# Optimization experiments

Measured on AMD Instinct MI355X. Metric: run time of the kernel, lower is better.

Reference implementation:

```python
import jax, jax.numpy as jnp
import numpy as np

VOCAB = 77
BLANK = VOCAB          # blank_index=-1 in tf.nn.ctc_greedy_decoder -> last class (77)
PRED_LEN = 30          # ctc_prediction_len


def _greedy_decode_row(best):
    """CTC greedy decode of one row. best: [T] int32 argmax path.
    Collapse consecutive repeats, drop blanks, pad to PRED_LEN with -1
    (matches tf.nn.ctc_greedy_decoder + sparse_to_dense(default=-1))."""
    prev = jnp.concatenate([jnp.full((1,), -1, best.dtype), best[:-1]])
    keep = (best != BLANK) & (best != prev)
    pos = jnp.cumsum(keep.astype(jnp.int32)) - 1
    # route dropped / overflow tokens to a scratch slot PRED_LEN
    pos = jnp.where(keep, jnp.minimum(pos, PRED_LEN), PRED_LEN)
    out = jnp.full((PRED_LEN + 1,), -1, jnp.int32).at[pos].set(best)
    return out[:PRED_LEN]


def setup_inputs() -> dict:
    key = jax.random.key(0)
    k1, k2, k3 = jax.random.split(key, 3)
    B, T, D = 1024, 80, 512
    feat_vec = jax.random.normal(k1, (B, T, D), jnp.float32)
    W = jax.random.normal(k2, (D, VOCAB + 1), jnp.float32) * (1.0 / np.sqrt(D))
    b = jnp.zeros((VOCAB + 1,), jnp.float32)
    y = jax.random.randint(k3, (B, PRED_LEN), 0, VOCAB)
    times = T
    return {"feat_vec": feat_vec, "W": W, "b": b, "y": y, "times": times}


def reference(feat_vec, W, b, y, times):
    # Dense classifier with softmax: [B, T, VOCAB+1]
    logits = jax.nn.softmax(jnp.einsum("btd,dc->btc", feat_vec, W) + b, axis=-1)
    # CTC greedy decode (merge_repeated=True), full sequence length = times = T
    best = jnp.argmax(logits, axis=-1).astype(jnp.int32)  # [B, T]
    res_lab = jax.vmap(_greedy_decode_row)(best)          # [B, PRED_LEN]
    return logits, res_lab
```

## Files before the change

### kernel.cpp

```cpp
#include <hip/hip_runtime.h>
#include <math.h>

#define B_     1024
#define T_     80
#define D_     512
#define C_     78
#define PRED_  30
#define BLANK_ 77
#define NKK    16
#define FRAG   512
#define PLANE_STRIDE (5 * NKK * FRAG)
#define ROWS_PB 160

typedef __attribute__((ext_vector_type(8))) _Float16 f16x8;
typedef __attribute__((ext_vector_type(4))) float    f32x4;

__device__ __forceinline__ void load_lds16(const void* g, void* l) {
    __builtin_amdgcn_global_load_lds(
        (const __attribute__((address_space(1))) unsigned int*)g,
        (__attribute__((address_space(3))) unsigned int*)l, 16, 0, 0);
}

__global__ __launch_bounds__(256) void prep_w(const float* __restrict__ W,
                                              ushort* __restrict__ Wf) {
    int i = blockIdx.x * 256 + threadIdx.x;
    if (i >= 2 * PLANE_STRIDE) return;
    int j    = i & 7;
    int lane = (i >> 3) & 63;
    int kk   = (i >> 9) & 15;
    int rest = i >> 13;
    int ct   = rest % 5;
    int plane = rest / 5;
    int q = lane >> 4, n = lane & 15;
    int k = kk * 32 + q * 8 + j;
    int c = ct * 16 + n;
    float v = (c < C_) ? W[k * C_ + c] : 0.f;
    _Float16 h1 = (_Float16)v;
    union { _Float16 h; ushort u; } cv;
    cv.h = (plane == 0) ? h1 : (_Float16)(v - (float)h1);
    Wf[i] = cv.u;
}

__global__ __launch_bounds__(320, 3) void gemm_ctc(
    const float* __restrict__ feat,
    const ushort* __restrict__ Wf,
    const float* __restrict__ bias,
    float* __restrict__ probs,
    float* __restrict__ lab)
{
    __shared__ __align__(16) float Abuf[2][ROWS_PB * 32];
    __shared__ int best_s[2][T_];

    const int tid  = threadIdx.x;
    const int w    = tid >> 6;
    const int lane = tid & 63;
    const int q    = lane >> 4;
    const int n    = lane & 15;

    f32x4 acc[2][5];
    #pragma unroll
    for (int t = 0; t < 2; ++t)
        #pragma unroll
        for (int ct = 0; ct < 5; ++ct)
            acc[t][ct] = (f32x4){0.f, 0.f, 0.f, 0.f};

    const float*  Abase = feat + (size_t)blockIdx.x * ROWS_PB * D_;
    const ushort* bp0   = Wf + lane * 8;

    auto stage = [&](int buf, int kk) {
        #pragma unroll
        for (int r = 0; r < 4; ++r) {
            int p   = r * 320 + w * 64 + lane;
            int row = p >> 3;
            int pc  = p & 7;
            int src = pc ^ (row & 7);
            const float* g = Abase + (size_t)row * D_ + kk * 32 + src * 4;
            float* l = &Abuf[buf][(size_t)(r * 320 + w * 64) * 4];
            load_lds16(g, l);
        }
    };

    stage(0, 0);
    int cur = 0;
    for (int kk = 0; kk < NKK; ++kk) {
        __syncthreads();
        if (kk < NKK - 1) stage(cur ^ 1, kk + 1);

        const float* Ab = &Abuf[cur][0];
        f16x8 a1f[2], a2f[2];
        #pragma unroll
        for (int t = 0; t < 2; ++t) {
            int rowl = w * 32 + t * 16 + n;
            int sw   = n & 7;
            float4 f0 = *(const float4*)(Ab + rowl * 32 + (((2 * q)     ^ sw) * 4));
            float4 f1 = *(const float4*)(Ab + rowl * 32 + (((2 * q + 1) ^ sw) * 4));
            float v[8] = {f0.x, f0.y, f0.z, f0.w, f1.x, f1.y, f1.z, f1.w};
            #pragma unroll
            for (int j = 0; j < 8; ++j) {
                _Float16 h = (_Float16)v[j];
                a1f[t][j] = h;
                a2f[t][j] = (_Float16)(v[j] - (float)h);
            }
        }
        #pragma unroll
        for (int ct = 0; ct < 5; ++ct) {
            const ushort* bp = bp0 + (ct * NKK + kk) * FRAG;
            f16x8 b1 = *(const f16x8*)bp;
            f16x8 b2 = *(const f16x8*)(bp + PLANE_STRIDE);
            acc[0][ct] = __builtin_amdgcn_mfma_f32_16x16x32_f16(a1f[0], b1, acc[0][ct], 0, 0, 0);
            acc[0][ct] = __builtin_amdgcn_mfma_f32_16x16x32_f16(a2f[0], b1, acc[0][ct], 0, 0, 0);
            acc[0][ct] = __builtin_amdgcn_mfma_f32_16x16x32_f16(a1f[0], b2, acc[0][ct], 0, 0, 0);
            acc[0][ct] = __builtin_amdgcn_mfma_f32_16x16x32_f16(a2f[0], b2, acc[0][ct], 0, 0, 0);
            acc[1][ct] = __builtin_amdgcn_mfma_f32_16x16x32_f16(a1f[1], b1, acc[1][ct], 0, 0, 0);
            acc[1][ct] = __builtin_amdgcn_mfma_f32_16x16x32_f16(a2f[1], b1, acc[1][ct], 0, 0, 0);
            acc[1][ct] = __builtin_amdgcn_mfma_f32_16x16x32_f16(a1f[1], b2, acc[1][ct], 0, 0, 0);
            acc[1][ct] = __builtin_amdgcn_mfma_f32_16x16x32_f16(a2f[1], b2, acc[1][ct], 0, 0, 0);
        }
        cur ^= 1;
    }

    #pragma unroll
    for (int t = 0; t < 2; ++t) {
        float x[5][4];
        #pragma unroll
        for (int ct = 0; ct < 5; ++ct) {
            int c = ct * 16 + n;
            bool valid = (c < C_);
            float bv = valid ? bias[c] : 0.f;
            #pragma unroll
            for (int r = 0; r < 4; ++r)
                x[ct][r] = valid ? (acc[t][ct][r] + bv) : -INFINITY;
        }
        float av[4]; int ai[4];
        #pragma unroll
        for (int r = 0; r < 4; ++r) {
            av[r] = x[0][r]; ai[r] = n;
            #pragma unroll
            for (int ct = 1; ct < 5; ++ct) {
                int c = ct * 16 + n;
                if (x[ct][r] > av[r]) { av[r] = x[ct][r]; ai[r] = c; }
            }
        }
        #pragma unroll
        for (int off = 8; off >= 1; off >>= 1) {
            #pragma unroll
            for (int r = 0; r < 4; ++r) {
                float ov = __shfl_xor(av[r], off, 16);
                int   oi = __shfl_xor(ai[r], off, 16);
                if (ov > av[r] || (ov == av[r] && oi < ai[r])) { av[r] = ov; ai[r] = oi; }
            }
        }
        float s[4] = {0.f, 0.f, 0.f, 0.f};
        #pragma unroll
        for (int ct = 0; ct < 5; ++ct)
            #pragma unroll
            for (int r = 0; r < 4; ++r) {
                x[ct][r] = __expf(x[ct][r] - av[r]);
                s[r] += x[ct][r];
            }
        #pragma unroll
        for (int off = 8; off >= 1; off >>= 1)
            #pragma unroll
            for (int r = 0; r < 4; ++r) s[r] += __shfl_xor(s[r], off, 16);

        const size_t growb = (size_t)blockIdx.x * ROWS_PB + w * 32 + t * 16 + q * 4;
        #pragma unroll
        for (int r = 0; r < 4; ++r) {
            float inv = 1.f / s[r];
            float* op = probs + (growb + r) * C_;
            #pragma unroll
            for (int ct = 0; ct < 5; ++ct) {
                int c = ct * 16 + n;
                if (c < C_) __builtin_nontemporal_store(x[ct][r] * inv, op + c);
            }
        }
        if (n == 0) {
            int rl = w * 32 + t * 16 + q * 4;
            #pragma unroll
            for (int r = 0; r < 4; ++r) {
                int rr = rl + r;
                best_s[rr / T_][rr % T_] = ai[r];
            }
        }
    }
    __syncthreads();

    if (tid < 2) {
        const int* bs = best_s[tid];
        float* op = lab + ((size_t)blockIdx.x * 2 + tid) * PRED_;
        int prev = -1, pos = 0;
        for (int t2 = 0; t2 < T_; ++t2) {
            int v = bs[t2];
            if (v != BLANK_ && v != prev) {
                if (pos < PRED_) op[pos] = (float)v;
                ++pos;
            }
            prev = v;
        }
        for (int i2 = (pos < PRED_ ? pos : PRED_); i2 < PRED_; ++i2) op[i2] = -1.f;
    }
}

extern "C" void kernel_launch(void* const* d_in, const int* in_sizes, int n_in,
                              void* d_out, int out_size, void* d_ws, size_t ws_size,
                              hipStream_t stream) {
    const float* feat = (const float*)d_in[0];
    const float* W    = (const float*)d_in[1];
    const float* bias = (const float*)d_in[2];
    float*  probs = (float*)d_out;
    float*  lab   = probs + (size_t)B_ * T_ * C_;
    ushort* Wf    = (ushort*)d_ws;

    hipLaunchKernelGGL(prep_w, dim3(320), dim3(256), 0, stream, W, Wf);
    hipLaunchKernelGGL(gemm_ctc, dim3(B_ / 2), dim3(320), 0, stream,
                       feat, Wf, bias, probs, lab);
}
```

Baseline: 263.2 us.

## Load A directly into registers, one sequence per block, drop lo*lo MFMA

Removes the LDS double-buffered staging of feature rows and instead has each lane load its A fragment straight from global memory with a one-step register prefetch. Each block now handles one sequence (80 rows, 16 per wave) instead of two, which doubles the grid and raises the occupancy hint. It also drops the low-times-low split-precision MFMA term, cutting matrix work by a quarter at a small accuracy cost. Without LDS staging, global loads are less coalesced (each lane reads 32 bytes across strided rows), and B fragments are reloaded per 16 rows instead of per 32.

```diff
diff --git a/kernel.cpp b/kernel.cpp
--- a/kernel.cpp
+++ b/kernel.cpp
@@ -10,16 +10,9 @@
 #define NKK    16
 #define FRAG   512
 #define PLANE_STRIDE (5 * NKK * FRAG)
-#define ROWS_PB 160
 
 typedef __attribute__((ext_vector_type(8))) _Float16 f16x8;
 typedef __attribute__((ext_vector_type(4))) float    f32x4;
-
-__device__ __forceinline__ void load_lds16(const void* g, void* l) {
-    __builtin_amdgcn_global_load_lds(
-        (const __attribute__((address_space(1))) unsigned int*)g,
-        (__attribute__((address_space(3))) unsigned int*)l, 16, 0, 0);
-}
 
 __global__ __launch_bounds__(256) void prep_w(const float* __restrict__ W,
                                               ushort* __restrict__ Wf) {
@@ -41,15 +34,14 @@
     Wf[i] = cv.u;
 }
 
-__global__ __launch_bounds__(320, 3) void gemm_ctc(
+__global__ __launch_bounds__(320, 4) void gemm_ctc(
     const float* __restrict__ feat,
     const ushort* __restrict__ Wf,
     const float* __restrict__ bias,
     float* __restrict__ probs,
     float* __restrict__ lab)
 {
-    __shared__ __align__(16) float Abuf[2][ROWS_PB * 32];
-    __shared__ int best_s[2][T_];
+    __shared__ int best_s[T_];
 
     const int tid  = threadIdx.x;
     const int w    = tid >> 6;
@@ -57,140 +49,111 @@
     const int q    = lane >> 4;
     const int n    = lane & 15;
 
-    f32x4 acc[2][5];
+    f32x4 acc[5];
     #pragma unroll
-    for (int t = 0; t < 2; ++t)
+    for (int ct = 0; ct < 5; ++ct)
+        acc[ct] = (f32x4){0.f, 0.f, 0.f, 0.f};
+
+    const float*  Ap  = feat + ((size_t)blockIdx.x * T_ + w * 16 + n) * D_ + q * 8;
+    const ushort* bp0 = Wf + lane * 8;
+
+    float4 c0 = *(const float4*)(Ap);
+    float4 c1 = *(const float4*)(Ap + 4);
+
+    #pragma unroll 2
+    for (int kk = 0; kk < NKK; ++kk) {
+        const int nk = (kk < NKK - 1) ? kk + 1 : NKK - 1;
+        float4 n0 = *(const float4*)(Ap + nk * 32);
+        float4 n1 = *(const float4*)(Ap + nk * 32 + 4);
+
+        float v[8] = {c0.x, c0.y, c0.z, c0.w, c1.x, c1.y, c1.z, c1.w};
+        f16x8 a1f, a2f;
         #pragma unroll
-        for (int ct = 0; ct < 5; ++ct)
-            acc[t][ct] = (f32x4){0.f, 0.f, 0.f, 0.f};
+        for (int j = 0; j < 8; ++j) {
+            _Float16 h = (_Float16)v[j];
+            a1f[j] = h;
+            a2f[j] = (_Float16)(v[j] - (float)h);
+        }
 
-    const float*  Abase = feat + (size_t)blockIdx.x * ROWS_PB * D_;
-    const ushort* bp0   = Wf + lane * 8;
+        const ushort* bpk = bp0 + kk * FRAG;
+        #pragma unroll
+        for (int ct = 0; ct < 5; ++ct) {
+            const ushort* bp = bpk + ct * (NKK * FRAG);
+            f16x8 b1 = *(const f16x8*)bp;
+            f16x8 b2 = *(const f16x8*)(bp + PLANE_STRIDE);
+            acc[ct] = __builtin_amdgcn_mfma_f32_16x16x32_f16(a1f, b1, acc[ct], 0, 0, 0);
+            acc[ct] = __builtin_amdgcn_mfma_f32_16x16x32_f16(a2f, b1, acc[ct], 0, 0, 0);
+            acc[ct] = __builtin_amdgcn_mfma_f32_16x16x32_f16(a1f, b2, acc[ct], 0, 0, 0);
+        }
+        c0 = n0; c1 = n1;
+    }
 
-    auto stage = [&](int buf, int kk) {
+    float x[5][4];
+    #pragma unroll
+    for (int ct = 0; ct < 5; ++ct) {
+        int c = ct * 16 + n;
+        bool valid = (c < C_);
+        float bv = valid ? bias[c] : 0.f;
+        #pragma unroll
+        for (int r = 0; r < 4; ++r)
+            x[ct][r] = valid ? (acc[ct][r] + bv) : -INFINITY;
+    }
+    float av[4]; int ai[4];
+    #pragma unroll
+    for (int r = 0; r < 4; ++r) {
+        av[r] = x[0][r]; ai[r] = n;
+        #pragma unroll
+        for (int ct = 1; ct < 5; ++ct) {
+            int c = ct * 16 + n;
+            if (x[ct][r] > av[r]) { av[r] = x[ct][r]; ai[r] = c; }
+        }
+    }
+    #pragma unroll
+    for (int off = 8; off >= 1; off >>= 1) {
         #pragma unroll
         for (int r = 0; r < 4; ++r) {
-            int p   = r * 320 + w * 64 + lane;
-            int row = p >> 3;
-            int pc  = p & 7;
-            int src = pc ^ (row & 7);
-            const float* g = Abase + (size_t)row * D_ + kk * 32 + src * 4;
-            float* l = &Abuf[buf][(size_t)(r * 320 + w * 64) * 4];
-            load_lds16(g, l);
+            float ov = __shfl_xor(av[r], off, 16);
+            int   oi = __shfl_xor(ai[r], off, 16);
+            if (ov > av[r] || (ov == av[r] && oi < ai[r])) { av[r] = ov; ai[r] = oi; }
         }
-    };
+    }
+    float s[4] = {0.f, 0.f, 0.f, 0.f};
+    #pragma unroll
+    for (int ct = 0; ct < 5; ++ct)
+        #pragma unroll
+        for (int r = 0; r < 4; ++r) {
+            x[ct][r] = __expf(x[ct][r] - av[r]);
+            s[r] += x[ct][r];
+        }
+    #pragma unroll
+    for (int off = 8; off >= 1; off >>= 1)
+        #pragma unroll
+        for (int r = 0; r < 4; ++r) s[r] += __shfl_xor(s[r], off, 16);
 
-    stage(0, 0);
-    int cur = 0;
-    for (int kk = 0; kk < NKK; ++kk) {
-        __syncthreads();
-        if (kk < NKK - 1) stage(cur ^ 1, kk + 1);
-
-        const float* Ab = &Abuf[cur][0];
-        f16x8 a1f[2], a2f[2];
-        #pragma unroll
-        for (int t = 0; t < 2; ++t) {
-            int rowl = w * 32 + t * 16 + n;
-            int sw   = n & 7;
-            float4 f0 = *(const float4*)(Ab + rowl * 32 + (((2 * q)     ^ sw) * 4));
-            float4 f1 = *(const float4*)(Ab + rowl * 32 + (((2 * q + 1) ^ sw) * 4));
-            float v[8] = {f0.x, f0.y, f0.z, f0.w, f1.x, f1.y, f1.z, f1.w};
-            #pragma unroll
-            for (int j = 0; j < 8; ++j) {
-                _Float16 h = (_Float16)v[j];
-                a1f[t][j] = h;
-                a2f[t][j] = (_Float16)(v[j] - (float)h);
-            }
-        }
-        #pragma unroll
-        for (int ct = 0; ct < 5; ++ct) {
-            const ushort* bp = bp0 + (ct * NKK + kk) * FRAG;
-            f16x8 b1 = *(const f16x8*)bp;
-            f16x8 b2 = *(const f16x8*)(bp + PLANE_STRIDE);
-            acc[0][ct] = __builtin_amdgcn_mfma_f32_16x16x32_f16(a1f[0], b1, acc[0][ct], 0, 0, 0);
-            acc[0][ct] = __builtin_amdgcn_mfma_f32_16x16x32_f16(a2f[0], b1, acc[0][ct], 0, 0, 0);
-            acc[0][ct] = __builtin_amdgcn_mfma_f32_16x16x32_f16(a1f[0], b2, acc[0][ct], 0, 0, 0);
-            acc[0][ct] = __builtin_amdgcn_mfma_f32_16x16x32_f16(a2f[0], b2, acc[0][ct], 0, 0, 0);
-            acc[1][ct] = __builtin_amdgcn_mfma_f32_16x16x32_f16(a1f[1], b1, acc[1][ct], 0, 0, 0);
-            acc[1][ct] = __builtin_amdgcn_mfma_f32_16x16x32_f16(a2f[1], b1, acc[1][ct], 0, 0, 0);
-            acc[1][ct] = __builtin_amdgcn_mfma_f32_16x16x32_f16(a1f[1], b2, acc[1][ct], 0, 0, 0);
-            acc[1][ct] = __builtin_amdgcn_mfma_f32_16x16x32_f16(a2f[1], b2, acc[1][ct], 0, 0, 0);
-        }
-        cur ^= 1;
-    }
-
+    const size_t growb = (size_t)blockIdx.x * T_ + w * 16 + q * 4;
     #pragma unroll
-    for (int t = 0; t < 2; ++t) {
-        float x[5][4];
+    for (int r = 0; r < 4; ++r) {
+        float inv = 1.f / s[r];
+        float* op = probs + (growb + r) * C_;
         #pragma unroll
         for (int ct = 0; ct < 5; ++ct) {
             int c = ct * 16 + n;
-            bool valid = (c < C_);
-            float bv = valid ? bias[c] : 0.f;
-            #pragma unroll
-            for (int r = 0; r < 4; ++r)
-                x[ct][r] = valid ? (acc[t][ct][r] + bv) : -INFINITY;
+            if (c < C_) __builtin_nontemporal_store(x[ct][r] * inv, op + c);
         }
-        float av[4]; int ai[4];
+    }
+    if (n == 0) {
+        int rl = w * 16 + q * 4;
         #pragma unroll
-        for (int r = 0; r < 4; ++r) {
-            av[r] = x[0][r]; ai[r] = n;
-            #pragma unroll
-            for (int ct = 1; ct < 5; ++ct) {
-                int c = ct * 16 + n;
-                if (x[ct][r] > av[r]) { av[r] = x[ct][r]; ai[r] = c; }
-            }
-        }
-        #pragma unroll
-        for (int off = 8; off >= 1; off >>= 1) {
-            #pragma unroll
-            for (int r = 0; r < 4; ++r) {
-                float ov = __shfl_xor(av[r], off, 16);
-                int   oi = __shfl_xor(ai[r], off, 16);
-                if (ov > av[r] || (ov == av[r] && oi < ai[r])) { av[r] = ov; ai[r] = oi; }
-            }
-        }
-        float s[4] = {0.f, 0.f, 0.f, 0.f};
-        #pragma unroll
-        for (int ct = 0; ct < 5; ++ct)
-            #pragma unroll
-            for (int r = 0; r < 4; ++r) {
-                x[ct][r] = __expf(x[ct][r] - av[r]);
-                s[r] += x[ct][r];
-            }
-        #pragma unroll
-        for (int off = 8; off >= 1; off >>= 1)
-            #pragma unroll
-            for (int r = 0; r < 4; ++r) s[r] += __shfl_xor(s[r], off, 16);
-
-        const size_t growb = (size_t)blockIdx.x * ROWS_PB + w * 32 + t * 16 + q * 4;
-        #pragma unroll
-        for (int r = 0; r < 4; ++r) {
-            float inv = 1.f / s[r];
-            float* op = probs + (growb + r) * C_;
-            #pragma unroll
-            for (int ct = 0; ct < 5; ++ct) {
-                int c = ct * 16 + n;
-                if (c < C_) __builtin_nontemporal_store(x[ct][r] * inv, op + c);
-            }
-        }
-        if (n == 0) {
-            int rl = w * 32 + t * 16 + q * 4;
-            #pragma unroll
-            for (int r = 0; r < 4; ++r) {
-                int rr = rl + r;
-                best_s[rr / T_][rr % T_] = ai[r];
-            }
-        }
+        for (int r = 0; r < 4; ++r)
+            best_s[rl + r] = ai[r];
     }
     __syncthreads();
 
-    if (tid < 2) {
-        const int* bs = best_s[tid];
-        float* op = lab + ((size_t)blockIdx.x * 2 + tid) * PRED_;
+    if (tid == 0) {
+        float* op = lab + (size_t)blockIdx.x * PRED_;
         int prev = -1, pos = 0;
         for (int t2 = 0; t2 < T_; ++t2) {
-            int v = bs[t2];
+            int v = best_s[t2];
             if (v != BLANK_ && v != prev) {
                 if (pos < PRED_) op[pos] = (float)v;
                 ++pos;
@@ -212,6 +175,6 @@
     ushort* Wf    = (ushort*)d_ws;
 
     hipLaunchKernelGGL(prep_w, dim3(320), dim3(256), 0, stream, W, Wf);
-    hipLaunchKernelGGL(gemm_ctc, dim3(B_ / 2), dim3(320), 0, stream,
+    hipLaunchKernelGGL(gemm_ctc, dim3(B_), dim3(320), 0, stream,
                        feat, Wf, bias, probs, lab);
 }
```

Result: slower. 284.5 us (+8.1%).

## Triple-buffer A and W fragments in LDS and drop lo*lo MFMA term

Applied to the files above, without the earlier changes.

W fragments are now staged into LDS alongside the feature tile through direct global-to-LDS loads, replacing per-wave global loads inside the K loop. The pipeline becomes triple-buffered, with explicit vmcnt waits and raw s_barrier instead of __syncthreads. The smallest split-fp16 correction product (a_lo*b_lo) is removed, cutting MFMAs by a quarter at a tiny accuracy cost. LDS use grows to about 92KB per block and the occupancy hint is removed, so far fewer blocks fit per CU, which may hurt latency hiding.

```diff
diff --git a/kernel.cpp b/kernel.cpp
--- a/kernel.cpp
+++ b/kernel.cpp
@@ -11,9 +11,13 @@
 #define FRAG   512
 #define PLANE_STRIDE (5 * NKK * FRAG)
 #define ROWS_PB 160
+#define A_BYTES (ROWS_PB * 128)
+#define SLICE_BYTES (A_BYTES + 10 * 1024)
 
 typedef __attribute__((ext_vector_type(8))) _Float16 f16x8;
 typedef __attribute__((ext_vector_type(4))) float    f32x4;
+
+#define WAITVM(N) asm volatile("s_waitcnt vmcnt(" #N ")" ::: "memory")
 
 __device__ __forceinline__ void load_lds16(const void* g, void* l) {
     __builtin_amdgcn_global_load_lds(
@@ -41,14 +45,14 @@
     Wf[i] = cv.u;
 }
 
-__global__ __launch_bounds__(320, 3) void gemm_ctc(
+__global__ __launch_bounds__(320) void gemm_ctc(
     const float* __restrict__ feat,
     const ushort* __restrict__ Wf,
     const float* __restrict__ bias,
     float* __restrict__ probs,
     float* __restrict__ lab)
 {
-    __shared__ __align__(16) float Abuf[2][ROWS_PB * 32];
+    __shared__ __align__(16) unsigned char Sbuf[3][SLICE_BYTES];
     __shared__ int best_s[2][T_];
 
     const int tid  = threadIdx.x;
@@ -57,6 +61,28 @@
     const int q    = lane >> 4;
     const int n    = lane & 15;
 
+    const float* Abase = feat + (size_t)blockIdx.x * ROWS_PB * D_;
+
+    auto stage = [&](int buf, int kk) {
+        #pragma unroll
+        for (int l = 0; l < 4; ++l) {
+            int rb  = w * 4 + l;
+            int row = rb * 8 + (lane >> 3);
+            int pc  = lane & 7;
+            int sc  = pc ^ (row & 7);
+            const float* g = Abase + (size_t)row * D_ + kk * 32 + sc * 4;
+            load_lds16(g, Sbuf[buf] + rb * 1024);
+        }
+        #pragma unroll
+        for (int f2 = 0; f2 < 2; ++f2) {
+            int f     = w * 2 + f2;
+            int plane = f / 5, ct = f % 5;
+            const ushort* g = Wf + (size_t)plane * PLANE_STRIDE
+                                 + (ct * NKK + kk) * FRAG + lane * 8;
+            load_lds16(g, Sbuf[buf] + A_BYTES + f * 1024);
+        }
+    };
+
     f32x4 acc[2][5];
     #pragma unroll
     for (int t = 0; t < 2; ++t)
@@ -64,29 +90,9 @@
         for (int ct = 0; ct < 5; ++ct)
             acc[t][ct] = (f32x4){0.f, 0.f, 0.f, 0.f};
 
-    const float*  Abase = feat + (size_t)blockIdx.x * ROWS_PB * D_;
-    const ushort* bp0   = Wf + lane * 8;
-
-    auto stage = [&](int buf, int kk) {
-        #pragma unroll
-        for (int r = 0; r < 4; ++r) {
-            int p   = r * 320 + w * 64 + lane;
-            int row = p >> 3;
-            int pc  = p & 7;
-            int src = pc ^ (row & 7);
-            const float* g = Abase + (size_t)row * D_ + kk * 32 + src * 4;
-            float* l = &Abuf[buf][(size_t)(r * 320 + w * 64) * 4];
-            load_lds16(g, l);
-        }
-    };
-
-    stage(0, 0);
-    int cur = 0;
-    for (int kk = 0; kk < NKK; ++kk) {
-        __syncthreads();
-        if (kk < NKK - 1) stage(cur ^ 1, kk + 1);
-
-        const float* Ab = &Abuf[cur][0];
+    auto body = [&](int buf) {
+        const float*  Ab = (const float*)(Sbuf[buf]);
+        const ushort* Bb = (const ushort*)(Sbuf[buf] + A_BYTES);
         f16x8 a1f[2], a2f[2];
         #pragma unroll
         for (int t = 0; t < 2; ++t) {
@@ -104,20 +110,29 @@
         }
         #pragma unroll
         for (int ct = 0; ct < 5; ++ct) {
-            const ushort* bp = bp0 + (ct * NKK + kk) * FRAG;
-            f16x8 b1 = *(const f16x8*)bp;
-            f16x8 b2 = *(const f16x8*)(bp + PLANE_STRIDE);
+            f16x8 b1 = *(const f16x8*)(Bb + ct * 512       + lane * 8);
+            f16x8 b2 = *(const f16x8*)(Bb + (5 + ct) * 512 + lane * 8);
             acc[0][ct] = __builtin_amdgcn_mfma_f32_16x16x32_f16(a1f[0], b1, acc[0][ct], 0, 0, 0);
             acc[0][ct] = __builtin_amdgcn_mfma_f32_16x16x32_f16(a2f[0], b1, acc[0][ct], 0, 0, 0);
             acc[0][ct] = __builtin_amdgcn_mfma_f32_16x16x32_f16(a1f[0], b2, acc[0][ct], 0, 0, 0);
-            acc[0][ct] = __builtin_amdgcn_mfma_f32_16x16x32_f16(a2f[0], b2, acc[0][ct], 0, 0, 0);
             acc[1][ct] = __builtin_amdgcn_mfma_f32_16x16x32_f16(a1f[1], b1, acc[1][ct], 0, 0, 0);
             acc[1][ct] = __builtin_amdgcn_mfma_f32_16x16x32_f16(a2f[1], b1, acc[1][ct], 0, 0, 0);
             acc[1][ct] = __builtin_amdgcn_mfma_f32_16x16x32_f16(a1f[1], b2, acc[1][ct], 0, 0, 0);
-            acc[1][ct] = __builtin_amdgcn_mfma_f32_16x16x32_f16(a2f[1], b2, acc[1][ct], 0, 0, 0);
-        }
-        cur ^= 1;
+        }
+    };
+
+    stage(0, 0);
+    stage(1, 1);
+
+    for (int kk = 0; kk < 15; ++kk) {
+        WAITVM(6);
+        __builtin_amdgcn_s_barrier();
+        if (kk <= 13) stage((kk + 2) % 3, kk + 2);
+        body(kk % 3);
     }
+    WAITVM(0);
+    __builtin_amdgcn_s_barrier();
+    body(0);
 
     #pragma unroll
     for (int t = 0; t < 2; ++t) {
```

Result: slower. 271.2 us (+3.1%).
